# Kernel tuning notes

Measured on AMD Instinct MI355X. Metric: run time of the kernel, lower is better.

Reference implementation:

```python
import jax, jax.numpy as jnp
import numpy as np

HEIGHT = 8
IN_DIM = 128
OUT_DIM = 8
BATCH = 65536
INT_NODES = 2 ** HEIGHT - 1   # 255
LEAF_NODES = 2 ** HEIGHT      # 256


def _and_weight(height):
    # Fixed +-1 structured routing matrix [leaf, int_nodes] (DGTreg._get_and_layer_params).
    leaf = 2 ** height
    w = np.zeros((leaf, leaf - 1), dtype=np.float32)
    for i in range(height):
        num = 2 ** i
        start = num - 1
        for j in range(start, start + num):
            rb = leaf // num * (j - start)
            rm = rb + leaf // (2 * num)
            re = rb + leaf // num
            w[rb:rm, j] = 1.0
            w[rm:re, j] = -1.0
    return jnp.asarray(w)


def setup_inputs() -> dict:
    key = jax.random.key(0)
    k = jax.random.split(key, 5)
    x = jax.random.normal(k[0], (BATCH, IN_DIM), jnp.float32)
    # orthogonal-ish predicate weight (scaled gaussian), zero bias per module init
    Wp = jax.random.normal(k[1], (INT_NODES, IN_DIM), jnp.float32) / np.sqrt(IN_DIM)
    bp = jnp.zeros((INT_NODES,), jnp.float32)
    Wand = _and_weight(HEIGHT)
    # xavier_uniform for or-layer weights [out_dim, in_dim, leaf]
    lim = np.sqrt(6.0 / (IN_DIM + LEAF_NODES)).astype(np.float32)
    Wor = jax.random.uniform(k[2], (OUT_DIM, IN_DIM, LEAF_NODES), jnp.float32, -lim, lim)
    bor = jax.random.normal(k[3], (OUT_DIM, IN_DIM), jnp.float32) * 0.01
    lim2 = np.sqrt(6.0 / (LEAF_NODES + OUT_DIM)).astype(np.float32)
    action_stds = jax.random.uniform(k[4], (LEAF_NODES, OUT_DIM), jnp.float32, -lim2, lim2)
    return {"x": x, "Wp": Wp, "bp": bp, "Wand": Wand, "Wor": Wor, "bor": bor,
            "action_stds": action_stds}


def reference(x, Wp, bp, Wand, Wor, bor, action_stds):
    sg = jax.lax.stop_gradient
    # predicate layer: [B, int_nodes]
    pred_z = x @ Wp.T + bp
    # ScaleBinarizer1: fac = mean(|z|) per row; binarize to {fac, 0}; straight-through grad
    fac = jnp.mean(jnp.abs(pred_z), axis=-1, keepdims=True)
    binz = jnp.where(pred_z >= 0, fac, 0.0)
    pred_a = pred_z + sg(binz - pred_z)          # forward = binz, grad = identity
    pred_a = 2.0 * pred_a - sg(fac)              # in {+fac, -fac}
    # fixed structured 'and' layer -> softmax over leaves
    and_z = pred_a @ Wand.T                      # [B, leaf]
    and_a = jax.nn.softmax(and_z, axis=-1)
    # Sparser1: keep only max entry per row, straight-through grad
    mx = jnp.max(and_a, axis=-1, keepdims=True)
    sp = jnp.where(and_a >= mx, and_a, 0.0)
    and_a = and_a + sg(sp - and_a)
    # or layers: per-output Linear(leaf->in_dim) then <wt, x>
    wt = jnp.einsum('bl,oil->boi', and_a, Wor) + bor[None]   # [B, out, in]
    out = jnp.einsum('boi,bi->bo', wt, x)                    # [B, out]
    # std head over detached routing weights
    std = jnp.sum(action_stds[None] * sg(and_a)[:, :, None], axis=1)  # [B, out]
    std = jnp.clip(std, -20.0, 2.0)
    return (out, std)
```

## Files before the change

kernel.cpp:

```cpp
#include <hip/hip_runtime.h>

#define BATCH 65536
#define IN_DIM 128
#define INT_NODES 255
#define LEAF 256
#define OUT_DIM 8
#define AMB_TH 1.5e-3f

typedef float    f4v __attribute__((ext_vector_type(4)));
typedef _Float16 h8v __attribute__((ext_vector_type(8)));
typedef _Float16 h2v __attribute__((ext_vector_type(2)));

#define LGKM0() __asm__ volatile("s_waitcnt lgkmcnt(0)" ::: "memory")

__device__ __align__(16) _Float16 g_Wh[LEAF * 1024];
__device__ __align__(16) _Float16 g_Bf[32768];
__device__ __align__(16) _Float16 g_Bb[2048];

__device__ __forceinline__ float fdot2(h2v a, h2v b, float c) {
#if __has_builtin(__builtin_amdgcn_fdot2)
    return __builtin_amdgcn_fdot2(a, b, c, false);
#else
    return c + (float)a[0] * (float)b[0] + (float)a[1] * (float)b[1];
#endif
}

__global__ __launch_bounds__(256) void prep(const float* __restrict__ Wor,
                                            const float* __restrict__ Wp,
                                            const float* __restrict__ bor) {
    if (blockIdx.x < 64) {
        __shared__ float t[64][65];
        const int rt = blockIdx.x >> 2, ct = blockIdx.x & 3;
        const int r0 = rt * 64, c0 = ct * 64;
        const int tx = threadIdx.x & 63, ty = threadIdx.x >> 6;
#pragma unroll
        for (int p = 0; p < 16; ++p) {
            int r = ty + p * 4;
            t[r][tx] = Wor[(size_t)(r0 + r) * 256 + c0 + tx];
        }
        __syncthreads();
#pragma unroll
        for (int p = 0; p < 16; ++p) {
            int r = ty + p * 4;
            g_Wh[(size_t)(c0 + r) * 1024 + r0 + tx] = (_Float16)t[tx][r];
        }
    } else if (blockIdx.x < 192) {
        int slot = (blockIdx.x - 64) * 256 + threadIdx.x;
        int j    = slot & 7;
        int lane = (slot >> 3) & 63;
        int ntg  = (slot >> 9) & 15;
        int ks   = slot >> 13;
        int n = ntg * 16 + (lane & 15);
        int k = ks * 32 + (lane >> 4) * 8 + j;
        float v = (n < INT_NODES) ? Wp[n * IN_DIM + k] : 0.f;
        g_Bf[slot] = (_Float16)v;
    } else {
        int slot = (blockIdx.x - 192) * 256 + threadIdx.x;
        int j    = slot & 7;
        int lane = (slot >> 3) & 63;
        int ks   = slot >> 9;
        int o = lane & 15;
        int k = ks * 32 + (lane >> 4) * 8 + j;
        float v = (o < OUT_DIM) ? bor[o * IN_DIM + k] : 0.f;
        g_Bb[slot] = (_Float16)v;
    }
}

__global__ __launch_bounds__(256) void dgt_main(
    const float* __restrict__ x, const float* __restrict__ Wp,
    const float* __restrict__ bp, const float* __restrict__ stds,
    float* __restrict__ out, float* __restrict__ stdo) {

    __shared__ unsigned char sgnS[4][LEAF * 4];
    __shared__ float asumS[4][16 * 16];
    __shared__ float hdS[4][16 * 36];
    __shared__ float tbS[4][16 * 8];
    __shared__ float psS[4][16];
    __shared__ int   lfS[4][16];

    const int tid  = threadIdx.x;
    const int wave = tid >> 6;
    const int lane = tid & 63;
    const int c = lane & 15;
    const int g = lane >> 4;
    const int rowbase = blockIdx.x * 64 + wave * 16;

    unsigned char* sgn = sgnS[wave];
    float* asum = asumS[wave];
    float* hd = hdS[wave];

    h8v ah[4];
    {
        const float* xb = x + (size_t)(rowbase + c) * IN_DIM;
#pragma unroll
        for (int ks = 0; ks < 4; ++ks) {
            const float* p = xb + ks * 32 + g * 8;
            float4 v0 = *reinterpret_cast<const float4*>(p);
            float4 v1 = *reinterpret_cast<const float4*>(p + 4);
            h8v a;
            a[0] = (_Float16)v0.x; a[1] = (_Float16)v0.y;
            a[2] = (_Float16)v0.z; a[3] = (_Float16)v0.w;
            a[4] = (_Float16)v1.x; a[5] = (_Float16)v1.y;
            a[6] = (_Float16)v1.z; a[7] = (_Float16)v1.w;
            ah[ks] = a;
        }
    }

    {
        const h8v* Bb8 = (const h8v*)g_Bb;
        f4v tb = (f4v){0.f, 0.f, 0.f, 0.f};
#pragma unroll
        for (int ks = 0; ks < 4; ++ks)
            tb = __builtin_amdgcn_mfma_f32_16x16x32_f16(ah[ks], Bb8[ks * 64 + lane], tb, 0, 0, 0);
        if (c < OUT_DIM) {
#pragma unroll
            for (int rr = 0; rr < 4; ++rr)
                tbS[wave][(g * 4 + rr) * 8 + c] = tb[rr];
        }
    }

    const h8v* Bf8 = (const h8v*)g_Bf;
    float pp[4] = {0.f, 0.f, 0.f, 0.f};
#pragma unroll
    for (int h = 0; h < 2; ++h) {
        f4v acc[8];
#pragma unroll
        for (int nt = 0; nt < 8; ++nt) acc[nt] = (f4v){0.f, 0.f, 0.f, 0.f};
#pragma unroll
        for (int ks = 0; ks < 4; ++ks)
#pragma unroll
            for (int nt = 0; nt < 8; ++nt) {
                h8v b = Bf8[(ks * 16 + h * 8 + nt) * 64 + lane];
                acc[nt] = __builtin_amdgcn_mfma_f32_16x16x32_f16(ah[ks], b, acc[nt], 0, 0, 0);
            }
#pragma unroll
        for (int nt = 0; nt < 8; ++nt) {
            const int n = h * 128 + nt * 16 + c;
            const float bpv = (n < INT_NODES) ? bp[n] : 0.f;
            unsigned by = 0;
#pragma unroll
            for (int rr = 0; rr < 4; ++rr) {
                float v = acc[nt][rr] + bpv;
                float av = fabsf(v);
                pp[rr] += av;
                by |= ((v < 0.f ? 1u : 0u) | (av < AMB_TH ? 2u : 0u)) << (2 * rr);
            }
            sgn[n * 4 + g] = (unsigned char)by;
        }
    }
#pragma unroll
    for (int rr = 0; rr < 4; ++rr) asum[(g * 4 + rr) * 16 + c] = pp[rr];

    h2v xh[16];
    {
        const float* xr = x + (size_t)(rowbase + (lane >> 2)) * IN_DIM;
        const int kq = lane & 3;
#pragma unroll
        for (int ch = 0; ch < 4; ++ch) {
            const int base = (ch * 4 + kq) * 8;
            float4 v0 = *reinterpret_cast<const float4*>(xr + base);
            float4 v1 = *reinterpret_cast<const float4*>(xr + base + 4);
            xh[ch * 4 + 0] = (h2v){(_Float16)v0.x, (_Float16)v0.y};
            xh[ch * 4 + 1] = (h2v){(_Float16)v0.z, (_Float16)v0.w};
            xh[ch * 4 + 2] = (h2v){(_Float16)v1.x, (_Float16)v1.y};
            xh[ch * 4 + 3] = (h2v){(_Float16)v1.z, (_Float16)v1.w};
        }
    }
    LGKM0();

    if (lane < 16) {
        const int r = lane;
        float s = 0.f;
#pragma unroll
        for (int cc = 0; cc < 16; cc += 4) {
            f4v v = *reinterpret_cast<f4v*>(&asum[r * 16 + cc]);
            s += (v[0] + v[1]) + (v[2] + v[3]);
        }
        const float fac = s * (1.0f / (float)INT_NODES);
        const float e = expf(-2.0f * fac);
        const float q = 1.0f + e;
        const float q2 = q * q, q4 = q2 * q2, q8 = q4 * q4;

        int node = 0;
#pragma unroll
        for (int d = 0; d < 8; ++d) {
            unsigned by = sgn[node * 4 + (r >> 2)];
            int code = (int)((by >> ((r & 3) * 2)) & 3u);
            int neg;
            if (code & 2) {
                const float* wr = Wp + node * IN_DIM;
                const float* xrow = x + (size_t)(rowbase + r) * IN_DIM;
                double z0 = 0.0, z1 = 0.0, z2 = 0.0, z3 = 0.0;
                for (int k = 0; k < IN_DIM; k += 4) {
                    float4 wv = *reinterpret_cast<const float4*>(wr + k);
                    float4 xv = *reinterpret_cast<const float4*>(xrow + k);
                    z0 = fma((double)wv.x, (double)xv.x, z0);
                    z1 = fma((double)wv.y, (double)xv.y, z1);
                    z2 = fma((double)wv.z, (double)xv.z, z2);
                    z3 = fma((double)wv.w, (double)xv.w, z3);
                }
                double zd = ((z0 + z1) + (z2 + z3)) + (double)bp[node];
                neg = (zd < 0.0) ? 1 : 0;
            } else {
                neg = code & 1;
            }
            node = 2 * node + 1 + neg;
        }
        psS[wave][r] = 1.0f / q8;
        lfS[wave][r] = node - INT_NODES;
    }
    LGKM0();

    {
        const int r = lane >> 2, kq = lane & 3;
        const int leaf = lfS[wave][r];
        const _Float16* wl = g_Wh + (size_t)leaf * 1024;
        float hp[8];
#pragma unroll
        for (int o = 0; o < 8; ++o) hp[o] = 0.f;
#pragma unroll
        for (int ch = 0; ch < 4; ++ch) {
            const int base = (ch * 4 + kq) * 8;
            h2v x0 = xh[ch * 4 + 0], x1 = xh[ch * 4 + 1];
            h2v x2 = xh[ch * 4 + 2], x3 = xh[ch * 4 + 3];
#pragma unroll
            for (int o = 0; o < 8; ++o) {
                h8v w8 = *reinterpret_cast<const h8v*>(wl + o * IN_DIM + base);
                h2v w0 = {w8[0], w8[1]}, w1 = {w8[2], w8[3]};
                h2v w2 = {w8[4], w8[5]}, w3 = {w8[6], w8[7]};
                hp[o] = fdot2(w0, x0, hp[o]);
                hp[o] = fdot2(w1, x1, hp[o]);
                hp[o] = fdot2(w2, x2, hp[o]);
                hp[o] = fdot2(w3, x3, hp[o]);
            }
        }
#pragma unroll
        for (int o = 0; o < 8; ++o)
            hd[r * 36 + o * 4 + kq] = hp[o];
    }
    LGKM0();

    {
        const int r = lane >> 2, op = lane & 3, o0 = op * 2;
        const float ps = psS[wave][r];
        f4v a = *reinterpret_cast<f4v*>(&hd[r * 36 + o0 * 4]);
        f4v b = *reinterpret_cast<f4v*>(&hd[r * 36 + o0 * 4 + 4]);
        float2 ov;
        ov.x = ps * ((a[0] + a[1]) + (a[2] + a[3])) + tbS[wave][r * 8 + o0];
        ov.y = ps * ((b[0] + b[1]) + (b[2] + b[3])) + tbS[wave][r * 8 + o0 + 1];
        const size_t ob = (size_t)(rowbase + r) * OUT_DIM + o0;
        *reinterpret_cast<float2*>(out + ob) = ov;
        const int leaf = lfS[wave][r];
        float2 sv;
        sv.x = fminf(fmaxf(ps * stds[leaf * OUT_DIM + o0],     -20.0f), 2.0f);
        sv.y = fminf(fmaxf(ps * stds[leaf * OUT_DIM + o0 + 1], -20.0f), 2.0f);
        *reinterpret_cast<float2*>(stdo + ob) = sv;
    }
}

extern "C" void kernel_launch(void* const* d_in, const int* in_sizes, int n_in,
                              void* d_out, int out_size, void* d_ws, size_t ws_size,
                              hipStream_t stream) {
    const float* x    = (const float*)d_in[0];
    const float* Wp   = (const float*)d_in[1];
    const float* bp   = (const float*)d_in[2];
    const float* Wor  = (const float*)d_in[4];
    const float* bor  = (const float*)d_in[5];
    const float* stds = (const float*)d_in[6];
    float* out = (float*)d_out;
    (void)d_ws; (void)ws_size;

    prep<<<200, 256, 0, stream>>>(Wor, Wp, bor);
    dgt_main<<<BATCH / 64, 256, 0, stream>>>(x, Wp, bp, stds,
                                             out, out + (size_t)BATCH * OUT_DIM);
}
```

Before: 112.5 us.

## Stage predicate weights through LDS with double-buffered global_load_lds shared across waves

Before this, each wave read the fp16 predicate weight fragments straight from global memory for its own MFMAs. Now the four waves cooperatively copy each K-chunk into a double-buffered LDS stage with direct global-to-LDS loads, and the load of the next chunk overlaps compute on the current one. All waves then read the shared fragments from LDS, which cuts redundant global/L2 traffic by four. It adds two block barriers per stage, hoists the bias loads into registers, and sets a minimum of 4 blocks per CU in the launch bounds. The cost is extra LDS and synchronisation that could limit occupancy.

```diff
diff --git a/kernel.cpp b/kernel.cpp
--- a/kernel.cpp
+++ b/kernel.cpp
@@ -66,11 +66,27 @@
     }
 }
 
-__global__ __launch_bounds__(256) void dgt_main(
+#define STAGE(chunk, buf) do {                                                  \
+    const int h_ = (chunk) >> 2, ks_ = (chunk) & 3;                             \
+    const int nt0_ = wave * 2;                                                  \
+    const _Float16* g0_ = g_Bf + (size_t)(((ks_ * 16 + h_ * 8 + nt0_) * 64 + lane) * 8); \
+    const _Float16* g1_ = g0_ + 64 * 8;                                         \
+    __builtin_amdgcn_global_load_lds(                                           \
+        (const __attribute__((address_space(1))) void*)g0_,                     \
+        (__attribute__((address_space(3))) void*)&stageS[(buf)][nt0_ * 512],    \
+        16, 0, 0);                                                              \
+    __builtin_amdgcn_global_load_lds(                                           \
+        (const __attribute__((address_space(1))) void*)g1_,                     \
+        (__attribute__((address_space(3))) void*)&stageS[(buf)][(nt0_ + 1) * 512], \
+        16, 0, 0);                                                              \
+} while (0)
+
+__global__ __launch_bounds__(256, 4) void dgt_main(
     const float* __restrict__ x, const float* __restrict__ Wp,
     const float* __restrict__ bp, const float* __restrict__ stds,
     float* __restrict__ out, float* __restrict__ stdo) {
 
+    __shared__ __align__(16) _Float16 stageS[2][4096];
     __shared__ unsigned char sgnS[4][LEAF * 4];
     __shared__ float asumS[4][16 * 16];
     __shared__ float hdS[4][16 * 36];
@@ -88,6 +104,15 @@
     unsigned char* sgn = sgnS[wave];
     float* asum = asumS[wave];
     float* hd = hdS[wave];
+
+    float bpv[2][8];
+#pragma unroll
+    for (int h2 = 0; h2 < 2; ++h2)
+#pragma unroll
+        for (int nt = 0; nt < 8; ++nt) {
+            const int n = h2 * 128 + nt * 16 + c;
+            bpv[h2][nt] = (n < INT_NODES) ? bp[n] : 0.f;
+        }
 
     h8v ah[4];
     {
@@ -119,34 +144,43 @@
         }
     }
 
-    const h8v* Bf8 = (const h8v*)g_Bf;
     float pp[4] = {0.f, 0.f, 0.f, 0.f};
-#pragma unroll
-    for (int h = 0; h < 2; ++h) {
-        f4v acc[8];
-#pragma unroll
-        for (int nt = 0; nt < 8; ++nt) acc[nt] = (f4v){0.f, 0.f, 0.f, 0.f};
-#pragma unroll
-        for (int ks = 0; ks < 4; ++ks)
+    f4v acc[8];
+    __asm__ volatile("s_waitcnt vmcnt(0)" ::: "memory");
+    STAGE(0, 0);
+#pragma unroll
+    for (int s = 0; s < 8; ++s) {
+        const int h = s >> 2, ks = s & 3;
+        if (s + 1 < 8) STAGE(s + 1, (s + 1) & 1);
+        if (s < 7) __asm__ volatile("s_waitcnt vmcnt(2)" ::: "memory");
+        else       __asm__ volatile("s_waitcnt vmcnt(0)" ::: "memory");
+        __builtin_amdgcn_s_barrier();
+        if (ks == 0) {
+#pragma unroll
+            for (int nt = 0; nt < 8; ++nt) acc[nt] = (f4v){0.f, 0.f, 0.f, 0.f};
+        }
+        const h8v* bufp = (const h8v*)stageS[s & 1];
+#pragma unroll
+        for (int nt = 0; nt < 8; ++nt)
+            acc[nt] = __builtin_amdgcn_mfma_f32_16x16x32_f16(ah[ks], bufp[nt * 64 + lane], acc[nt], 0, 0, 0);
+        if (ks == 3) {
 #pragma unroll
             for (int nt = 0; nt < 8; ++nt) {
-                h8v b = Bf8[(ks * 16 + h * 8 + nt) * 64 + lane];
-                acc[nt] = __builtin_amdgcn_mfma_f32_16x16x32_f16(ah[ks], b, acc[nt], 0, 0, 0);
+                const int n = h * 128 + nt * 16 + c;
+                const float bpvv = bpv[h][nt];
+                unsigned by = 0;
+#pragma unroll
+                for (int rr = 0; rr < 4; ++rr) {
+                    float v = acc[nt][rr] + bpvv;
+                    float av = fabsf(v);
+                    pp[rr] += av;
+                    by |= ((v < 0.f ? 1u : 0u) | (av < AMB_TH ? 2u : 0u)) << (2 * rr);
+                }
+                sgn[n * 4 + g] = (unsigned char)by;
             }
-#pragma unroll
-        for (int nt = 0; nt < 8; ++nt) {
-            const int n = h * 128 + nt * 16 + c;
-            const float bpv = (n < INT_NODES) ? bp[n] : 0.f;
-            unsigned by = 0;
-#pragma unroll
-            for (int rr = 0; rr < 4; ++rr) {
-                float v = acc[nt][rr] + bpv;
-                float av = fabsf(v);
-                pp[rr] += av;
-                by |= ((v < 0.f ? 1u : 0u) | (av < AMB_TH ? 2u : 0u)) << (2 * rr);
-            }
-            sgn[n * 4 + g] = (unsigned char)by;
-        }
+        }
+        __asm__ volatile("s_waitcnt lgkmcnt(0)" ::: "memory");
+        __builtin_amdgcn_s_barrier();
     }
 #pragma unroll
     for (int rr = 0; rr < 4; ++rr) asum[(g * 4 + rr) * 16 + c] = pp[rr];
```

Result: no change. 111.1 us (-1.2%).
